# Kernel optimization log

Hardware: AMD Instinct MI355X
Metric: run time of the kernel (lower is better)

## Reference

```python
import jax, jax.numpy as jnp
import numpy as np

B, T, V, E, H = 4096, 16, 512, 512, 1024


def setup_inputs() -> dict:
    key = jax.random.key(0)
    ks = jax.random.split(key, 8)
    s = 0.05  # weight init scale
    return {
        "encoded_input": jax.random.normal(ks[0], (B, H), jnp.float32),
        "target": jax.random.randint(ks[1], (B, T), 0, V, jnp.int32),
        "emb": jax.random.normal(ks[2], (V, E), jnp.float32) * s,
        "W_ih": jax.random.normal(ks[3], (4 * H, E), jnp.float32) * s,
        "W_hh": jax.random.normal(ks[4], (4 * H, H), jnp.float32) * s,
        "b_ih": jax.random.normal(ks[5], (4 * H,), jnp.float32) * s,
        "b_hh": jax.random.normal(ks[6], (4 * H,), jnp.float32) * s,
        "W_out": jax.random.normal(ks[7], (V, H), jnp.float32) * s,
    }


def reference(encoded_input, target, emb, W_ih, W_hh, b_ih, b_hh, W_out):
    # Teacher-forced char LSTM decoder. Dropout(0.1) is identity in eval mode.
    b, t = target.shape
    # input char ids: start token 0, then shifted targets
    inp_ids = jnp.concatenate(
        [jnp.zeros((b, 1), target.dtype), target[:, :-1]], axis=1)  # [B,T]
    x = emb[inp_ids]  # [B,T,E]
    # precompute input contribution to gates for all steps
    xg = jnp.einsum('bte,ge->btg', x, W_ih) + b_ih + b_hh  # [B,T,4H]

    def step(carry, xs):
        h, c = carry
        xg_t, tgt_t = xs  # [B,4H], [B]
        gates = xg_t + h @ W_hh.T  # [B,4H]
        i, f, g, o = jnp.split(gates, 4, axis=-1)  # torch order i,f,g,o
        i = jax.nn.sigmoid(i)
        f = jax.nn.sigmoid(f)
        g = jnp.tanh(g)
        o = jax.nn.sigmoid(o)
        c = f * c + i * g
        h = o * jnp.tanh(c)
        logits = h @ W_out.T  # [B,V]
        # NLL of log_softmax at target index, expressed stably
        lse = jax.nn.logsumexp(logits, axis=-1)
        tgt_logit = jnp.take_along_axis(logits, tgt_t[:, None], axis=1)[:, 0]
        loss_t = lse - tgt_logit  # [B]
        return (h, c), loss_t

    h0 = encoded_input  # hidden = (encoded, encoded) for 1 layer
    (_, _), losses = jax.lax.scan(
        step, (h0, h0),
        (jnp.swapaxes(xg, 0, 1), target.T))  # scan over time: [T,B,...]
    return losses.sum(axis=0) / t  # [B] per-example mean loss
```

## Files before the change

kernel.cpp:

```cpp
#include <hip/hip_runtime.h>
#include <hip/hip_bf16.h>
#include <stdint.h>

typedef __attribute__((ext_vector_type(8))) short bf16x8;
typedef __attribute__((ext_vector_type(4))) float f32x4;

#define DEV __device__ __forceinline__
#define MFMA16(a, b, c) __builtin_amdgcn_mfma_f32_16x16x32_bf16(a, b, c, 0, 0, 0)

static constexpr int Bn = 4096;
static constexpr int Tn = 16;
static constexpr int Vn = 512;
static constexpr int En = 512;
static constexpr int Hn = 1024;
static constexpr int G4 = 4096;
static constexpr int KX = En + Hn;

DEV unsigned short f2bf(float f) {
    union { float f; uint32_t u; } v; v.f = f;
    return (unsigned short)((v.u + 0x7fffu + ((v.u >> 16) & 1u)) >> 16);
}
DEV float bf2f(unsigned short h) {
    union { uint32_t u; float f; } v; v.u = (uint32_t)h << 16; return v.f;
}
DEV float sigmoidf_(float x) { return 1.f / (1.f + __expf(-x)); }
DEV float tanhf_(float x)    { return 1.f - 2.f / (1.f + __expf(2.f * x)); }

DEV bf16x8 cvt8(const float* p) {
    f32x4 a = *(const f32x4*)p;
    f32x4 b = *(const f32x4*)(p + 4);
    bf16x8 o;
    o[0] = (short)f2bf(a[0]); o[1] = (short)f2bf(a[1]);
    o[2] = (short)f2bf(a[2]); o[3] = (short)f2bf(a[3]);
    o[4] = (short)f2bf(b[0]); o[5] = (short)f2bf(b[1]);
    o[6] = (short)f2bf(b[2]); o[7] = (short)f2bf(b[3]);
    return o;
}

__launch_bounds__(512, 2)
__global__ void lstm8(const unsigned short* __restrict__ Whp8,
                      const unsigned short* __restrict__ Hin,
                      const float* __restrict__ EGb,
                      const int* __restrict__ target, int t,
                      float* __restrict__ CstF,
                      unsigned short* __restrict__ Hout)
{
    __shared__ __align__(16) unsigned short lds[65536];

    const int tid = threadIdx.x;
    const int l   = tid & 63;
    const int w   = tid >> 6;
    const int wm  = w >> 2, wn = w & 3;
    const int q   = l >> 4, c15 = l & 15;
    const int bx  = blockIdx.x, by = blockIdx.y;
    const int n0  = bx * 256;

    const int cB = (((l & 7) ^ (l >> 3)) << 3);

    const int sw0   = ((q ^ (c15 & 7)) << 3);
    const int offA0 = c15 * 64 + sw0;
    const int offB0 = ((wn & 1) * 64 + c15) * 64 + sw0;

    f32x4 acc[8][4];
#pragma unroll
    for (int i = 0; i < 8; i++)
#pragma unroll
        for (int j = 0; j < 4; j++) acc[i][j] = f32x4{0.f, 0.f, 0.f, 0.f};

    auto stageA = [&](int kts, int cbuf) {
        const unsigned short* page =
            Whp8 + (((size_t)(by * 16 + kts) * 2) << 13);
#pragma unroll
        for (int h = 0; h < 2; h++)
#pragma unroll
            for (int L = 0; L < 2; L++) {
                const unsigned short* src =
                    page + h * 8192 + L * 4096 + w * 512 + l * 8;
                unsigned short* dst =
                    &lds[cbuf * 16384 + h * 8192 + L * 4096 + w * 512];
                __builtin_amdgcn_global_load_lds(
                    (const __attribute__((address_space(1))) uint32_t*)src,
                    (__attribute__((address_space(3))) uint32_t*)dst, 16, 0, 0);
            }
    };
    auto stageB = [&](int kts, int cbuf) {
#pragma unroll
        for (int h = 0; h < 2; h++)
#pragma unroll
            for (int L = 0; L < 2; L++) {
                const unsigned short* src =
                    Hin + (size_t)(n0 + h * 128 + L * 64 + w * 8 + (l >> 3)) * Hn
                        + kts * 64 + cB;
                unsigned short* dst =
                    &lds[32768 + cbuf * 16384 + h * 8192 + L * 4096 + w * 512];
                __builtin_amdgcn_global_load_lds(
                    (const __attribute__((address_space(1))) uint32_t*)src,
                    (__attribute__((address_space(3))) uint32_t*)dst, 16, 0, 0);
            }
    };

    stageA(0, 0); stageB(0, 0);
    stageA(1, 1); stageB(1, 1);
    asm volatile("s_waitcnt vmcnt(8)" ::: "memory");
    __builtin_amdgcn_s_barrier();

#pragma unroll 2
    for (int kt = 0; kt < 16; kt++) {
        const int cur = kt & 1;
        const unsigned short* Ab = &lds[cur * 16384 + wm * 8192];
        const unsigned short* Bb = &lds[32768 + cur * 16384 + (wn >> 1) * 8192];
        bf16x8 aF[8], bF[4];

#pragma unroll
        for (int i = 0; i < 8; i++)
            aF[i] = *(const bf16x8*)&Ab[offA0 + i * 1024];
#pragma unroll
        for (int j = 0; j < 4; j++)
            bF[j] = *(const bf16x8*)&Bb[offB0 + j * 1024];
        __builtin_amdgcn_s_setprio(1);
#pragma unroll
        for (int i = 0; i < 8; i++)
#pragma unroll
            for (int j = 0; j < 4; j++)
                acc[i][j] = MFMA16(aF[i], bF[j], acc[i][j]);
        __builtin_amdgcn_s_setprio(0);

#pragma unroll
        for (int i = 0; i < 8; i++)
            aF[i] = *(const bf16x8*)&Ab[(offA0 ^ 32) + i * 1024];
#pragma unroll
        for (int j = 0; j < 4; j++)
            bF[j] = *(const bf16x8*)&Bb[(offB0 ^ 32) + j * 1024];
        __builtin_amdgcn_s_setprio(1);
#pragma unroll
        for (int i = 0; i < 8; i++)
#pragma unroll
            for (int j = 0; j < 4; j++)
                acc[i][j] = MFMA16(aF[i], bF[j], acc[i][j]);
        __builtin_amdgcn_s_setprio(0);
        __builtin_amdgcn_s_barrier();

        const int kts = (kt + 2 < 16) ? (kt + 2) : 15;
        stageA(kts, cur);
        stageB(kts, cur);
        asm volatile("s_waitcnt vmcnt(8)" ::: "memory");
        __builtin_amdgcn_s_barrier();
    }

    int ids[4];
#pragma unroll
    for (int j = 0; j < 4; j++)
        ids[j] = (t > 0)
            ? target[(size_t)(n0 + wn * 64 + j * 16 + c15) * Tn + (t - 1)] : 0;

    const int U0 = by * 64;
    unsigned short* sH = &lds[32768];
#pragma unroll
    for (int i = 0; i < 8; i++) {
        const int Uloc = wm * 32 + i * 4 + q;
#pragma unroll
        for (int j = 0; j < 4; j++) {
            f32x4 eg = *(const f32x4*)&EGb[(size_t)ids[j] * G4 + (U0 + Uloc) * 4];
            float ig = sigmoidf_(acc[i][j][0] + eg[0]);
            float fg = sigmoidf_(acc[i][j][1] + eg[1]);
            float gg = tanhf_  (acc[i][j][2] + eg[2]);
            float og = sigmoidf_(acc[i][j][3] + eg[3]);
            const size_t cidx =
                ((((size_t)(by * 16 + bx) * 8 + w) * 32 + i * 4 + j) << 6) + l;
            float cOld = CstF[cidx];
            float cNew = fg * cOld + ig * gg;
            float h    = og * tanhf_(cNew);
            CstF[cidx] = cNew;
            const int bl = wn * 64 + j * 16 + c15;
            sH[bl * 64 + (Uloc ^ ((bl & 7) << 3))] = f2bf(h);
        }
    }
    __builtin_amdgcn_s_barrier();
    {
        const int row = tid >> 1;
        const int hs  = tid & 1;
        const int sx  = row & 7;
        size_t go = (size_t)(n0 + row) * Hn + U0 + hs * 32;
#pragma unroll
        for (int s = 0; s < 4; s++) {
            const int slog = hs * 4 + s;
            bf16x8 v = *(const bf16x8*)&sH[row * 64 + ((slog ^ sx) << 3)];
            *(bf16x8*)&Hout[go + s * 8] = v;
        }
    }
}

template <int BM, int BN, int EPI>
__launch_bounds__(256, 2)
__global__ void gemm_k(const unsigned short* __restrict__ A, int lda,
                       const unsigned short* __restrict__ Bw, int ldb,
                       int K,
                       const float* __restrict__ biasp,
                       float* __restrict__ Out,
                       unsigned short* __restrict__ Outb, int ldo)
{
    constexpr int BK = 32;
    constexpr int WM = BM / 2, WN = BN / 2;
    constexpr int MI = WM / 16, NJ = WN / 16;

    __shared__ __align__(16) unsigned short sA[BM * BK];
    __shared__ __align__(16) unsigned short sB[BN * BK];

    const int tid = threadIdx.x;
    const int l   = tid & 63;
    const int w   = tid >> 6;
    const int wm  = w >> 1, wn = w & 1;
    const int m0  = blockIdx.y * BM;
    const int n0  = blockIdx.x * BN;

    f32x4 acc[MI][NJ];
#pragma unroll
    for (int i = 0; i < MI; i++)
#pragma unroll
        for (int j = 0; j < NJ; j++) acc[i][j] = f32x4{0.f, 0.f, 0.f, 0.f};

    const int srow = l >> 2;
    const int scol = (l & 3) * 8;
    const int q    = l >> 4;
    const int c15  = l & 15;

    for (int k0 = 0; k0 < K; k0 += BK) {
#pragma unroll
        for (int c = 0; c < BM / 64; c++) {
            const unsigned short* src =
                A + (size_t)(m0 + c * 64 + w * 16 + srow) * lda + k0 + scol;
            unsigned short* dst = &sA[(c * 64 + w * 16) * BK];
            __builtin_amdgcn_global_load_lds(
                (const __attribute__((address_space(1))) uint32_t*)src,
                (__attribute__((address_space(3))) uint32_t*)dst, 16, 0, 0);
        }
#pragma unroll
        for (int c = 0; c < BN / 64; c++) {
            const unsigned short* src =
                Bw + (size_t)(n0 + c * 64 + w * 16 + srow) * ldb + k0 + scol;
            unsigned short* dst = &sB[(c * 64 + w * 16) * BK];
            __builtin_amdgcn_global_load_lds(
                (const __attribute__((address_space(1))) uint32_t*)src,
                (__attribute__((address_space(3))) uint32_t*)dst, 16, 0, 0);
        }
        __syncthreads();

        bf16x8 aF[MI], bF[NJ];
#pragma unroll
        for (int i = 0; i < MI; i++)
            aF[i] = *(const bf16x8*)&sA[(wm * WM + i * 16 + c15) * BK + q * 8];
#pragma unroll
        for (int j = 0; j < NJ; j++)
            bF[j] = *(const bf16x8*)&sB[(wn * WN + j * 16 + c15) * BK + q * 8];
#pragma unroll
        for (int i = 0; i < MI; i++)
#pragma unroll
            for (int j = 0; j < NJ; j++)
                acc[i][j] = MFMA16(aF[i], bF[j], acc[i][j]);
        __syncthreads();
    }

#pragma unroll
    for (int j = 0; j < NJ; j++) {
        const int colp = n0 + wn * WN + j * 16 + c15;
        const float bj = biasp ? biasp[colp] : 0.f;
#pragma unroll
        for (int i = 0; i < MI; i++) {
            const size_t rb = (size_t)(m0 + wm * WM + i * 16 + 4 * q);
#pragma unroll
            for (int r = 0; r < 4; r++) {
                float vv = acc[i][j][r] + bj;
                if constexpr (EPI == 0) Out[(rb + r) * ldo + colp] = vv;
                else Outb[(rb + r) * ldo + colp] = f2bf(vv);
            }
        }
    }
}

__launch_bounds__(512, 4)
__global__ void logits_lse(const unsigned short* __restrict__ A,
                           const unsigned short* __restrict__ Wob,
                           const int* __restrict__ target,
                           float* __restrict__ lossT)
{
    constexpr int BK = 32;
    __shared__ __align__(16) unsigned short sA[64 * BK];
    __shared__ __align__(16) unsigned short sB[512 * BK];
    __shared__ float redS[8 * 64];
    __shared__ float redT[8 * 64];
    __shared__ int   tgL[64];

    const int tid = threadIdx.x;
    const int l   = tid & 63;
    const int w   = tid >> 6;
    const int q   = l >> 4, c15 = l & 15;
    const int ra0 = blockIdx.x * 64;

    if (tid < 64) {
        int ra = ra0 + tid;
        tgL[tid] = target[(size_t)(ra & (Bn - 1)) * Tn + (ra >> 12)];
    }

    f32x4 acc[4][4];
#pragma unroll
    for (int i = 0; i < 4; i++)
#pragma unroll
        for (int j = 0; j < 4; j++) acc[i][j] = f32x4{0.f, 0.f, 0.f, 0.f};

    const int srow = l >> 2;
    const int scol = (l & 3) * 8;

    for (int k0 = 0; k0 < Hn; k0 += BK) {
#pragma unroll
        for (int c = 0; c < 4; c++) {
            const unsigned short* src =
                Wob + (size_t)(w * 64 + c * 16 + srow) * Hn + k0 + scol;
            unsigned short* dst = &sB[(w * 64 + c * 16) * BK];
            __builtin_amdgcn_global_load_lds(
                (const __attribute__((address_space(1))) uint32_t*)src,
                (__attribute__((address_space(3))) uint32_t*)dst, 16, 0, 0);
        }
        if (w < 4) {
            const unsigned short* src =
                A + (size_t)(ra0 + w * 16 + srow) * Hn + k0 + scol;
            unsigned short* dst = &sA[(w * 16) * BK];
            __builtin_amdgcn_global_load_lds(
                (const __attribute__((address_space(1))) uint32_t*)src,
                (__attribute__((address_space(3))) uint32_t*)dst, 16, 0, 0);
        }
        __syncthreads();

        bf16x8 aF[4], bF[4];
#pragma unroll
        for (int i = 0; i < 4; i++)
            aF[i] = *(const bf16x8*)&sA[(i * 16 + c15) * BK + q * 8];
#pragma unroll
        for (int j = 0; j < 4; j++)
            bF[j] = *(const bf16x8*)&sB[(w * 64 + j * 16 + c15) * BK + q * 8];
#pragma unroll
        for (int i = 0; i < 4; i++)
#pragma unroll
            for (int j = 0; j < 4; j++)
                acc[i][j] = MFMA16(aF[i], bF[j], acc[i][j]);
        __syncthreads();
    }

#pragma unroll
    for (int i = 0; i < 4; i++)
#pragma unroll
        for (int rr = 0; rr < 4; rr++) {
            const int rloc = i * 16 + q * 4 + rr;
            const int tg = tgL[rloc];
            float ps = 0.f, tv = 0.f;
#pragma unroll
            for (int j = 0; j < 4; j++) {
                float v = acc[i][j][rr];
                ps += __expf(v);
                int col = w * 64 + j * 16 + c15;
                tv += (col == tg) ? v : 0.f;
            }
#pragma unroll
            for (int d = 1; d < 16; d <<= 1) {
                ps += __shfl_xor(ps, d);
                tv += __shfl_xor(tv, d);
            }
            if (c15 == 0) {
                redS[w * 64 + rloc] = ps;
                redT[w * 64 + rloc] = tv;
            }
        }
    __syncthreads();
    if (tid < 64) {
        float se = 0.f, tv = 0.f;
#pragma unroll
        for (int w8 = 0; w8 < 8; w8++) {
            se += redS[w8 * 64 + tid];
            tv += redT[w8 * 64 + tid];
        }
        lossT[ra0 + tid] = __logf(se) - tv;
    }
}

__global__ void prep_w(const float* __restrict__ Wih,
                       const float* __restrict__ Whh,
                       unsigned short* __restrict__ Wp)
{
    int i = blockIdx.x * 256 + threadIdx.x;
    int n = i / 192, kc = (i % 192) * 8;
    int g = n & 3, u = n >> 2;
    const float* src = (kc < En) ? (Wih + (size_t)(g * Hn + u) * En + kc)
                                 : (Whh + (size_t)(g * Hn + u) * Hn + (kc - En));
    *(bf16x8*)&Wp[(size_t)n * KX + kc] = cvt8(src);
}

__global__ void prep_w8(const float* __restrict__ Whh,
                        unsigned short* __restrict__ Whp8)
{
    int idx = blockIdx.x * 256 + threadIdx.x;
    int o = idx * 8;
    int p = o & 8191;
    int h = (o >> 13) & 1;
    int kt = (o >> 14) & 15;
    int by = o >> 18;
    int r = p >> 6;
    int slot = (p & 63) >> 3;
    int cl = ((slot ^ (r & 7)) << 3);
    int n = by * 256 + h * 128 + r;
    int g = n & 3, u = n >> 2;
    *(bf16x8*)&Whp8[o] = cvt8(Whh + (size_t)(g * Hn + u) * Hn + kt * 64 + cl);
}

__global__ void prep_bias(const float* __restrict__ bih,
                          const float* __restrict__ bhh,
                          float* __restrict__ biasp)
{
    int n = blockIdx.x * 256 + threadIdx.x;
    int g = n & 3, u = n >> 2;
    biasp[n] = bih[g * Hn + u] + bhh[g * Hn + u];
}

__global__ void prep_wout(const float* __restrict__ Wout,
                          unsigned short* __restrict__ Wob)
{
    int i = blockIdx.x * 256 + threadIdx.x;
    size_t off = (size_t)i * 8;
    *(bf16x8*)&Wob[off] = cvt8(Wout + off);
}

__global__ void prep_emb(const float* __restrict__ emb,
                         unsigned short* __restrict__ embb)
{
    int i = blockIdx.x * 256 + threadIdx.x;
    size_t off = (size_t)i * 8;
    *(bf16x8*)&embb[off] = cvt8(emb + off);
}

__global__ void init_state(const float* __restrict__ enc,
                           float* __restrict__ CstF,
                           unsigned short* __restrict__ Xh0,
                           float* __restrict__ loss)
{
    int f = blockIdx.x * 256 + threadIdx.x;
    int l = f & 63, q = l >> 4, c15 = l & 15;
    int ij = (f >> 6) & 31, i = ij >> 2, j = ij & 3;
    int w = (f >> 11) & 7, wm = w >> 2, wn = w & 3;
    int bx = (f >> 14) & 15, by = (f >> 18) & 15;
    int b = bx * 256 + wn * 64 + j * 16 + c15;
    int U = by * 64 + wm * 32 + i * 4 + q;
    CstF[f] = enc[(size_t)b * Hn + U];
    if (f < Bn * Hn / 8) {
        int m = f >> 7, u8 = (f & 127) * 8;
        *(bf16x8*)&Xh0[(size_t)m * Hn + u8] = cvt8(enc + (size_t)m * Hn + u8);
    }
    if (f < Bn) loss[f] = 0.f;
}

__global__ void lse_k(const unsigned short* __restrict__ lg,
                      const int* __restrict__ target, int t,
                      float* __restrict__ lossOut)
{
    int w = threadIdx.x >> 6, l = threadIdx.x & 63;
    int ra = blockIdx.x * 4 + w;
    const unsigned short* row = lg + (size_t)ra * Vn;
    bf16x8 v = *(const bf16x8*)&row[l * 8];
    float x0 = bf2f((unsigned short)v[0]), x1 = bf2f((unsigned short)v[1]);
    float x2 = bf2f((unsigned short)v[2]), x3 = bf2f((unsigned short)v[3]);
    float x4 = bf2f((unsigned short)v[4]), x5 = bf2f((unsigned short)v[5]);
    float x6 = bf2f((unsigned short)v[6]), x7 = bf2f((unsigned short)v[7]);
    float mx = fmaxf(fmaxf(fmaxf(x0, x1), fmaxf(x2, x3)),
                     fmaxf(fmaxf(x4, x5), fmaxf(x6, x7)));
#pragma unroll
    for (int d = 1; d < 64; d <<= 1) mx = fmaxf(mx, __shfl_xor(mx, d));
    float se = __expf(x0 - mx) + __expf(x1 - mx) + __expf(x2 - mx) +
               __expf(x3 - mx) + __expf(x4 - mx) + __expf(x5 - mx) +
               __expf(x6 - mx) + __expf(x7 - mx);
#pragma unroll
    for (int d = 1; d < 64; d <<= 1) se += __shfl_xor(se, d);
    if (l == 0) {
        int tg = target[(size_t)ra * Tn + t];
        lossOut[ra] += (mx + __logf(se)) - bf2f(row[tg]);
    }
}

__global__ void finalize_b(const float* __restrict__ lossT,
                           float* __restrict__ out)
{
    int m = blockIdx.x * 256 + threadIdx.x;
    float s = 0.f;
#pragma unroll
    for (int k = 0; k < 16; k++) s += lossT[(size_t)k * Bn + m];
    out[m] = s * (1.f / 16.f);
}

__global__ void finalize_s(const float* __restrict__ loss,
                           float* __restrict__ out)
{
    int m = blockIdx.x * 256 + threadIdx.x;
    out[m] = loss[m] * (1.f / 16.f);
}

extern "C" void kernel_launch(void* const* d_in, const int* in_sizes, int n_in,
                              void* d_out, int out_size, void* d_ws, size_t ws_size,
                              hipStream_t stream)
{
    const float* enc    = (const float*)d_in[0];
    const int*   target = (const int*)d_in[1];
    const float* emb    = (const float*)d_in[2];
    const float* Wih    = (const float*)d_in[3];
    const float* Whh    = (const float*)d_in[4];
    const float* bih    = (const float*)d_in[5];
    const float* bhh    = (const float*)d_in[6];
    const float* Wout   = (const float*)d_in[7];
    float* out = (float*)d_out;
    (void)in_sizes; (void)n_in; (void)out_size;

    constexpr size_t SZ_Wp    = (size_t)G4 * KX * 2;
    constexpr size_t SZ_Whp8  = (size_t)G4 * Hn * 2;
    constexpr size_t SZ_Wob   = (size_t)Vn * Hn * 2;
    constexpr size_t SZ_biasp = (size_t)G4 * 4;
    constexpr size_t SZ_embb  = (size_t)Vn * En * 2;
    constexpr size_t SZ_EGb   = (size_t)Vn * G4 * 4;
    constexpr size_t SZ_Cst   = (size_t)Bn * Hn * 4;
    constexpr size_t SZ_H     = (size_t)Bn * Hn * 2;
    constexpr size_t SZ_LGS   = (size_t)Bn * Vn * 2;
    constexpr size_t SZ_LT    = (size_t)Bn * Tn * 4;
    auto pad = [](size_t b) { return (b + 255) & ~(size_t)255; };
    const size_t fixed = pad(SZ_Wp) + pad(SZ_Whp8) + pad(SZ_Wob) +
                         pad(SZ_biasp) + pad(SZ_embb) + pad(SZ_EGb) + pad(SZ_Cst);
    const size_t needB = fixed + 17 * pad(SZ_H) + pad(SZ_LGS) + pad(SZ_LT);
    const bool batched = ws_size >= needB;

    size_t off = 0;
    char* base = (char*)d_ws;
    auto alloc = [&](size_t bytes) -> void* {
        void* p = base + off; off += pad(bytes); return p;
    };
    unsigned short* Wp    = (unsigned short*)alloc(SZ_Wp);
    unsigned short* Whp8  = (unsigned short*)alloc(SZ_Whp8);
    unsigned short* Wob   = (unsigned short*)alloc(SZ_Wob);
    float*          biasp = (float*)alloc(SZ_biasp);
    unsigned short* embb  = (unsigned short*)alloc(SZ_embb);
    float*          EGb   = (float*)alloc(SZ_EGb);
    float*          CstF  = (float*)alloc(SZ_Cst);
    const int nslot = batched ? 17 : 3;
    unsigned short* Hs    = (unsigned short*)alloc((size_t)nslot * pad(SZ_H));
    unsigned short* lgS   = (unsigned short*)alloc(SZ_LGS);
    float*          lossT = (float*)alloc(batched ? SZ_LT : (size_t)Bn * 4);
    const size_t HSLOT = pad(SZ_H) / 2;

    prep_w    <<<3072, 256, 0, stream>>>(Wih, Whh, Wp);
    prep_w8   <<<2048, 256, 0, stream>>>(Whh, Whp8);
    prep_bias <<<16,   256, 0, stream>>>(bih, bhh, biasp);
    prep_wout <<<256,  256, 0, stream>>>(Wout, Wob);
    prep_emb  <<<128,  256, 0, stream>>>(emb, embb);
    init_state<<<16384, 256, 0, stream>>>(enc, CstF, Hs, lossT);

    gemm_k<128, 128, 0><<<dim3(32, 4), 256, 0, stream>>>(
        embb, En, Wp, KX, En, biasp, EGb, nullptr, G4);

    for (int t = 0; t < Tn; t++) {
        unsigned short* hIn  = Hs + (size_t)(batched ? t : (t % 3)) * HSLOT;
        unsigned short* hOut = Hs + (size_t)(batched ? (t + 1) : ((t + 1) % 3)) * HSLOT;
        lstm8<<<dim3(16, 16), 512, 0, stream>>>(
            Whp8, hIn, EGb, target, t, CstF, hOut);
        if (!batched) {
            gemm_k<128, 64, 2><<<dim3(8, 32), 256, 0, stream>>>(
                hOut, Hn, Wob, Hn, Hn, nullptr, nullptr, lgS, Vn);
            lse_k<<<1024, 256, 0, stream>>>(lgS, target, t, lossT);
        }
    }

    if (batched) {
        logits_lse<<<1024, 512, 0, stream>>>(Hs + HSLOT, Wob, target, lossT);
        finalize_b<<<16, 256, 0, stream>>>(lossT, out);
    } else {
        finalize_s<<<16, 256, 0, stream>>>(lossT, out);
    }
}
```

Baseline: 900.2 us.

## Interleave LSTM recurrent GEMM into four phases with staggered async LDS loads

The recurrent W_hh·h GEMM main loop in the LSTM step kernel is split into four sub-tile MFMA phases. Each phase issues part of the next tile's global-to-LDS loads (A one step ahead, B two steps ahead) between barriers, so memory traffic overlaps compute more finely. Register use drops because only half the A and B fragments are live at a time. The cost is many more barriers per k-step and a more fragile buffer-reuse ordering. The other kernels only get a load macro refactor.

```diff
diff --git a/kernel.cpp b/kernel.cpp
--- a/kernel.cpp
+++ b/kernel.cpp
@@ -37,6 +37,10 @@
     return o;
 }
 
+#define GLOAD16(s, d) __builtin_amdgcn_global_load_lds( \
+    (const __attribute__((address_space(1))) uint32_t*)(s), \
+    (__attribute__((address_space(3))) uint32_t*)(d), 16, 0, 0)
+
 __launch_bounds__(512, 2)
 __global__ void lstm8(const unsigned short* __restrict__ Whp8,
                       const unsigned short* __restrict__ Hin,
@@ -56,7 +60,6 @@
     const int n0  = bx * 256;
 
     const int cB = (((l & 7) ^ (l >> 3)) << 3);
-
     const int sw0   = ((q ^ (c15 & 7)) << 3);
     const int offA0 = c15 * 64 + sw0;
     const int offB0 = ((wn & 1) * 64 + c15) * 64 + sw0;
@@ -67,83 +70,113 @@
 #pragma unroll
         for (int j = 0; j < 4; j++) acc[i][j] = f32x4{0.f, 0.f, 0.f, 0.f};
 
-    auto stageA = [&](int kts, int cbuf) {
+    auto stA = [&](int kts, int cbuf, int h) {
         const unsigned short* page =
             Whp8 + (((size_t)(by * 16 + kts) * 2) << 13);
 #pragma unroll
-        for (int h = 0; h < 2; h++)
-#pragma unroll
-            for (int L = 0; L < 2; L++) {
-                const unsigned short* src =
-                    page + h * 8192 + L * 4096 + w * 512 + l * 8;
-                unsigned short* dst =
-                    &lds[cbuf * 16384 + h * 8192 + L * 4096 + w * 512];
-                __builtin_amdgcn_global_load_lds(
-                    (const __attribute__((address_space(1))) uint32_t*)src,
-                    (__attribute__((address_space(3))) uint32_t*)dst, 16, 0, 0);
-            }
+        for (int L = 0; L < 2; L++)
+            GLOAD16(page + h * 8192 + L * 4096 + w * 512 + l * 8,
+                    &lds[cbuf * 16384 + h * 8192 + L * 4096 + w * 512]);
     };
-    auto stageB = [&](int kts, int cbuf) {
-#pragma unroll
-        for (int h = 0; h < 2; h++)
-#pragma unroll
-            for (int L = 0; L < 2; L++) {
-                const unsigned short* src =
-                    Hin + (size_t)(n0 + h * 128 + L * 64 + w * 8 + (l >> 3)) * Hn
-                        + kts * 64 + cB;
-                unsigned short* dst =
-                    &lds[32768 + cbuf * 16384 + h * 8192 + L * 4096 + w * 512];
-                __builtin_amdgcn_global_load_lds(
-                    (const __attribute__((address_space(1))) uint32_t*)src,
-                    (__attribute__((address_space(3))) uint32_t*)dst, 16, 0, 0);
-            }
+    auto stB = [&](int kts, int cbuf, int h) {
+#pragma unroll
+        for (int L = 0; L < 2; L++)
+            GLOAD16(Hin + (size_t)(n0 + h * 128 + L * 64 + w * 8 + (l >> 3)) * Hn
+                        + kts * 64 + cB,
+                    &lds[32768 + cbuf * 16384 + h * 8192 + L * 4096 + w * 512]);
     };
 
-    stageA(0, 0); stageB(0, 0);
-    stageA(1, 1); stageB(1, 1);
-    asm volatile("s_waitcnt vmcnt(8)" ::: "memory");
+    stA(0, 0, 0); stA(0, 0, 1); stB(0, 0, 0); stB(0, 0, 1);
+    stB(1, 1, 0); stB(1, 1, 1);
+    asm volatile("s_waitcnt vmcnt(4)" ::: "memory");
     __builtin_amdgcn_s_barrier();
 
-#pragma unroll 2
+    bf16x8 aF[4][2], bF[4][2];
+
     for (int kt = 0; kt < 16; kt++) {
         const int cur = kt & 1;
         const unsigned short* Ab = &lds[cur * 16384 + wm * 8192];
         const unsigned short* Bb = &lds[32768 + cur * 16384 + (wn >> 1) * 8192];
-        bf16x8 aF[8], bF[4];
-
-#pragma unroll
-        for (int i = 0; i < 8; i++)
-            aF[i] = *(const bf16x8*)&Ab[offA0 + i * 1024];
-#pragma unroll
-        for (int j = 0; j < 4; j++)
-            bF[j] = *(const bf16x8*)&Bb[offB0 + j * 1024];
+        const int ktA = (kt + 1 < 16) ? kt + 1 : 15;
+        const int ktB = (kt + 2 < 16) ? kt + 2 : 15;
+
+#pragma unroll
+        for (int i = 0; i < 4; i++) {
+            aF[i][0] = *(const bf16x8*)&Ab[offA0 + i * 1024];
+            aF[i][1] = *(const bf16x8*)&Ab[(offA0 ^ 32) + i * 1024];
+        }
+#pragma unroll
+        for (int j = 0; j < 2; j++) {
+            bF[j][0] = *(const bf16x8*)&Bb[offB0 + j * 1024];
+            bF[j][1] = *(const bf16x8*)&Bb[(offB0 ^ 32) + j * 1024];
+        }
+        stA(ktA, cur ^ 1, 0);
+        __builtin_amdgcn_s_barrier();
+        asm volatile("s_waitcnt lgkmcnt(0)" ::: "memory");
+        __builtin_amdgcn_sched_barrier(0);
         __builtin_amdgcn_s_setprio(1);
 #pragma unroll
-        for (int i = 0; i < 8; i++)
-#pragma unroll
-            for (int j = 0; j < 4; j++)
-                acc[i][j] = MFMA16(aF[i], bF[j], acc[i][j]);
+        for (int i = 0; i < 4; i++)
+#pragma unroll
+            for (int j = 0; j < 2; j++) {
+                acc[i][j] = MFMA16(aF[i][0], bF[j][0], acc[i][j]);
+                acc[i][j] = MFMA16(aF[i][1], bF[j][1], acc[i][j]);
+            }
         __builtin_amdgcn_s_setprio(0);
-
-#pragma unroll
-        for (int i = 0; i < 8; i++)
-            aF[i] = *(const bf16x8*)&Ab[(offA0 ^ 32) + i * 1024];
-#pragma unroll
-        for (int j = 0; j < 4; j++)
-            bF[j] = *(const bf16x8*)&Bb[(offB0 ^ 32) + j * 1024];
+        __builtin_amdgcn_s_barrier();
+
+#pragma unroll
+        for (int j = 2; j < 4; j++) {
+            bF[j][0] = *(const bf16x8*)&Bb[offB0 + j * 1024];
+            bF[j][1] = *(const bf16x8*)&Bb[(offB0 ^ 32) + j * 1024];
+        }
+        stA(ktA, cur ^ 1, 1);
+        __builtin_amdgcn_s_barrier();
+        asm volatile("s_waitcnt lgkmcnt(0)" ::: "memory");
+        __builtin_amdgcn_sched_barrier(0);
         __builtin_amdgcn_s_setprio(1);
 #pragma unroll
-        for (int i = 0; i < 8; i++)
-#pragma unroll
-            for (int j = 0; j < 4; j++)
-                acc[i][j] = MFMA16(aF[i], bF[j], acc[i][j]);
+        for (int i = 0; i < 4; i++)
+#pragma unroll
+            for (int j = 2; j < 4; j++) {
+                acc[i][j] = MFMA16(aF[i][0], bF[j][0], acc[i][j]);
+                acc[i][j] = MFMA16(aF[i][1], bF[j][1], acc[i][j]);
+            }
         __builtin_amdgcn_s_setprio(0);
         __builtin_amdgcn_s_barrier();
 
-        const int kts = (kt + 2 < 16) ? (kt + 2) : 15;
-        stageA(kts, cur);
-        stageB(kts, cur);
-        asm volatile("s_waitcnt vmcnt(8)" ::: "memory");
+#pragma unroll
+        for (int i = 0; i < 4; i++) {
+            aF[i][0] = *(const bf16x8*)&Ab[offA0 + (i + 4) * 1024];
+            aF[i][1] = *(const bf16x8*)&Ab[(offA0 ^ 32) + (i + 4) * 1024];
+        }
+        stB(ktB, cur, 0);
+        __builtin_amdgcn_s_barrier();
+        asm volatile("s_waitcnt lgkmcnt(0)" ::: "memory");
+        __builtin_amdgcn_sched_barrier(0);
+        __builtin_amdgcn_s_setprio(1);
+#pragma unroll
+        for (int i = 0; i < 4; i++)
+#pragma unroll
+            for (int j = 0; j < 2; j++) {
+                acc[i + 4][j] = MFMA16(aF[i][0], bF[j][0], acc[i + 4][j]);
+                acc[i + 4][j] = MFMA16(aF[i][1], bF[j][1], acc[i + 4][j]);
+            }
+        __builtin_amdgcn_s_setprio(0);
+        __builtin_amdgcn_s_barrier();
+
+        stB(ktB, cur, 1);
+        __builtin_amdgcn_s_barrier();
+        __builtin_amdgcn_s_setprio(1);
+#pragma unroll
+        for (int i = 0; i < 4; i++)
+#pragma unroll
+            for (int j = 2; j < 4; j++) {
+                acc[i + 4][j] = MFMA16(aF[i][0], bF[j][0], acc[i + 4][j]);
+                acc[i + 4][j] = MFMA16(aF[i][1], bF[j][1], acc[i + 4][j]);
+            }
+        __builtin_amdgcn_s_setprio(0);
+        asm volatile("s_waitcnt vmcnt(4)" ::: "memory");
         __builtin_amdgcn_s_barrier();
     }
 
@@ -175,7 +208,7 @@
             sH[bl * 64 + (Uloc ^ ((bl & 7) << 3))] = f2bf(h);
         }
     }
-    __builtin_amdgcn_s_barrier();
+    __syncthreads();
     {
         const int row = tid >> 1;
         const int hs  = tid & 1;
@@ -230,18 +263,14 @@
             const unsigned short* src =
                 A + (size_t)(m0 + c * 64 + w * 16 + srow) * lda + k0 + scol;
             unsigned short* dst = &sA[(c * 64 + w * 16) * BK];
-            __builtin_amdgcn_global_load_lds(
-                (const __attribute__((address_space(1))) uint32_t*)src,
-                (__attribute__((address_space(3))) uint32_t*)dst, 16, 0, 0);
+            GLOAD16(src, dst);
         }
 #pragma unroll
         for (int c = 0; c < BN / 64; c++) {
             const unsigned short* src =
                 Bw + (size_t)(n0 + c * 64 + w * 16 + srow) * ldb + k0 + scol;
             unsigned short* dst = &sB[(c * 64 + w * 16) * BK];
-            __builtin_amdgcn_global_load_lds(
-                (const __attribute__((address_space(1))) uint32_t*)src,
-                (__attribute__((address_space(3))) uint32_t*)dst, 16, 0, 0);
+            GLOAD16(src, dst);
         }
         __syncthreads();
 
@@ -316,17 +345,13 @@
             const unsigned short* src =
                 Wob + (size_t)(w * 64 + c * 16 + srow) * Hn + k0 + scol;
             unsigned short* dst = &sB[(w * 64 + c * 16) * BK];
-            __builtin_amdgcn_global_load_lds(
-                (const __attribute__((address_space(1))) uint32_t*)src,
-                (__attribute__((address_space(3))) uint32_t*)dst, 16, 0, 0);
+            GLOAD16(src, dst);
         }
         if (w < 4) {
             const unsigned short* src =
                 A + (size_t)(ra0 + w * 16 + srow) * Hn + k0 + scol;
             unsigned short* dst = &sA[(w * 16) * BK];
-            __builtin_amdgcn_global_load_lds(
-                (const __attribute__((address_space(1))) uint32_t*)src,
-                (__attribute__((address_space(3))) uint32_t*)dst, 16, 0, 0);
+            GLOAD16(src, dst);
         }
         __syncthreads();
 
```

Measured after the change: 908.5 us. Within noise of the previous version (+0.9%).

## Fuse LSTM timesteps into persistent kernel with grid barrier; swizzle logits LDS

Applied to the files above, without the earlier changes.

Replaces the 16 per-timestep lstm8 launches with one persistent lstm16 kernel of 256 blocks that loops over time and synchronises through an atomic grid-wide barrier. This removes launch gaps and tail effects between steps. The batched logits kernel now reads a pre-swizzled W_out layout and uses a rotated column mapping to cut LDS bank conflicts. The input-weight prep is also shrunk to pack only W_ih, since the W_hh half was never used. The grid barrier relies on all 256 blocks being co-resident and could deadlock otherwise, and the spin-wait adds some per-step overhead.

```diff
diff --git a/kernel.cpp b/kernel.cpp
--- a/kernel.cpp
+++ b/kernel.cpp
@@ -14,7 +14,6 @@
 static constexpr int En = 512;
 static constexpr int Hn = 1024;
 static constexpr int G4 = 4096;
-static constexpr int KX = En + Hn;
 
 DEV unsigned short f2bf(float f) {
     union { float f; uint32_t u; } v; v.f = f;
@@ -37,16 +36,42 @@
     return o;
 }
 
-__launch_bounds__(512, 2)
-__global__ void lstm8(const unsigned short* __restrict__ Whp8,
-                      const unsigned short* __restrict__ Hin,
-                      const float* __restrict__ EGb,
-                      const int* __restrict__ target, int t,
-                      float* __restrict__ CstF,
-                      unsigned short* __restrict__ Hout)
-{
-    __shared__ __align__(16) unsigned short lds[65536];
-
+#define GLOAD16(s, d) __builtin_amdgcn_global_load_lds( \
+    (const __attribute__((address_space(1))) uint32_t*)(s), \
+    (__attribute__((address_space(3))) uint32_t*)(d), 16, 0, 0)
+
+DEV void grid_barrier(unsigned* bar)
+{
+    __syncthreads();
+    if (threadIdx.x == 0) {
+        __threadfence();
+        unsigned g = __hip_atomic_load(&bar[1], __ATOMIC_RELAXED,
+                                       __HIP_MEMORY_SCOPE_AGENT);
+        unsigned a = __hip_atomic_fetch_add(&bar[0], 1u, __ATOMIC_ACQ_REL,
+                                            __HIP_MEMORY_SCOPE_AGENT);
+        if (a == 255u) {
+            __hip_atomic_store(&bar[0], 0u, __ATOMIC_RELAXED,
+                               __HIP_MEMORY_SCOPE_AGENT);
+            __hip_atomic_store(&bar[1], g + 1u, __ATOMIC_RELEASE,
+                               __HIP_MEMORY_SCOPE_AGENT);
+        } else {
+            while (__hip_atomic_load(&bar[1], __ATOMIC_ACQUIRE,
+                                     __HIP_MEMORY_SCOPE_AGENT) == g)
+                __builtin_amdgcn_s_sleep(2);
+        }
+        __threadfence();
+    }
+    __syncthreads();
+}
+
+DEV void lstm_step(unsigned short* lds,
+                   const unsigned short* __restrict__ Whp8,
+                   const unsigned short* __restrict__ Hin,
+                   const float* __restrict__ EGb,
+                   const int* __restrict__ target, int t,
+                   float* __restrict__ CstF,
+                   unsigned short* __restrict__ Hout)
+{
     const int tid = threadIdx.x;
     const int l   = tid & 63;
     const int w   = tid >> 6;
@@ -55,8 +80,7 @@
     const int bx  = blockIdx.x, by = blockIdx.y;
     const int n0  = bx * 256;
 
-    const int cB = (((l & 7) ^ (l >> 3)) << 3);
-
+    const int cB    = (((l & 7) ^ (l >> 3)) << 3);
     const int sw0   = ((q ^ (c15 & 7)) << 3);
     const int offA0 = c15 * 64 + sw0;
     const int offB0 = ((wn & 1) * 64 + c15) * 64 + sw0;
@@ -67,40 +91,28 @@
 #pragma unroll
         for (int j = 0; j < 4; j++) acc[i][j] = f32x4{0.f, 0.f, 0.f, 0.f};
 
-    auto stageA = [&](int kts, int cbuf) {
+    auto stA = [&](int kts, int cbuf) {
         const unsigned short* page =
             Whp8 + (((size_t)(by * 16 + kts) * 2) << 13);
 #pragma unroll
         for (int h = 0; h < 2; h++)
 #pragma unroll
-            for (int L = 0; L < 2; L++) {
-                const unsigned short* src =
-                    page + h * 8192 + L * 4096 + w * 512 + l * 8;
-                unsigned short* dst =
-                    &lds[cbuf * 16384 + h * 8192 + L * 4096 + w * 512];
-                __builtin_amdgcn_global_load_lds(
-                    (const __attribute__((address_space(1))) uint32_t*)src,
-                    (__attribute__((address_space(3))) uint32_t*)dst, 16, 0, 0);
-            }
+            for (int L = 0; L < 2; L++)
+                GLOAD16(page + h * 8192 + L * 4096 + w * 512 + l * 8,
+                        &lds[cbuf * 16384 + h * 8192 + L * 4096 + w * 512]);
     };
-    auto stageB = [&](int kts, int cbuf) {
+    auto stB = [&](int kts, int cbuf) {
 #pragma unroll
         for (int h = 0; h < 2; h++)
 #pragma unroll
-            for (int L = 0; L < 2; L++) {
-                const unsigned short* src =
-                    Hin + (size_t)(n0 + h * 128 + L * 64 + w * 8 + (l >> 3)) * Hn
-                        + kts * 64 + cB;
-                unsigned short* dst =
-                    &lds[32768 + cbuf * 16384 + h * 8192 + L * 4096 + w * 512];
-                __builtin_amdgcn_global_load_lds(
-                    (const __attribute__((address_space(1))) uint32_t*)src,
-                    (__attribute__((address_space(3))) uint32_t*)dst, 16, 0, 0);
-            }
+            for (int L = 0; L < 2; L++)
+                GLOAD16(Hin + (size_t)(n0 + h * 128 + L * 64 + w * 8 + (l >> 3)) * Hn
+                            + kts * 64 + cB,
+                        &lds[32768 + cbuf * 16384 + h * 8192 + L * 4096 + w * 512]);
     };
 
-    stageA(0, 0); stageB(0, 0);
-    stageA(1, 1); stageB(1, 1);
+    stA(0, 0); stB(0, 0);
+    stA(1, 1); stB(1, 1);
     asm volatile("s_waitcnt vmcnt(8)" ::: "memory");
     __builtin_amdgcn_s_barrier();
 
@@ -141,8 +153,8 @@
         __builtin_amdgcn_s_barrier();
 
         const int kts = (kt + 2 < 16) ? (kt + 2) : 15;
-        stageA(kts, cur);
-        stageB(kts, cur);
+        stA(kts, cur);
+        stB(kts, cur);
         asm volatile("s_waitcnt vmcnt(8)" ::: "memory");
         __builtin_amdgcn_s_barrier();
     }
@@ -175,7 +187,7 @@
             sH[bl * 64 + (Uloc ^ ((bl & 7) << 3))] = f2bf(h);
         }
     }
-    __builtin_amdgcn_s_barrier();
+    __syncthreads();
     {
         const int row = tid >> 1;
         const int hs  = tid & 1;
@@ -188,6 +200,34 @@
             *(bf16x8*)&Hout[go + s * 8] = v;
         }
     }
+}
+
+__launch_bounds__(512, 2)
+__global__ void lstm16(const unsigned short* __restrict__ Whp8,
+                       unsigned short* __restrict__ Hs, size_t HSLOT,
+                       const float* __restrict__ EGb,
+                       const int* __restrict__ target,
+                       float* __restrict__ CstF,
+                       unsigned* __restrict__ bar)
+{
+    __shared__ __align__(16) unsigned short lds[65536];
+    for (int t = 0; t < Tn; t++) {
+        lstm_step(lds, Whp8, Hs + (size_t)t * HSLOT, EGb, target, t, CstF,
+                  Hs + (size_t)(t + 1) * HSLOT);
+        if (t + 1 < Tn) grid_barrier(bar);
+    }
+}
+
+__launch_bounds__(512, 2)
+__global__ void lstm8(const unsigned short* __restrict__ Whp8,
+                      const unsigned short* __restrict__ Hin,
+                      const float* __restrict__ EGb,
+                      const int* __restrict__ target, int t,
+                      float* __restrict__ CstF,
+                      unsigned short* __restrict__ Hout)
+{
+    __shared__ __align__(16) unsigned short lds[65536];
+    lstm_step(lds, Whp8, Hin, EGb, target, t, CstF, Hout);
 }
 
 template <int BM, int BN, int EPI>
@@ -226,23 +266,13 @@
 
     for (int k0 = 0; k0 < K; k0 += BK) {
 #pragma unroll
-        for (int c = 0; c < BM / 64; c++) {
-            const unsigned short* src =
-                A + (size_t)(m0 + c * 64 + w * 16 + srow) * lda + k0 + scol;
-            unsigned short* dst = &sA[(c * 64 + w * 16) * BK];
-            __builtin_amdgcn_global_load_lds(
-                (const __attribute__((address_space(1))) uint32_t*)src,
-                (__attribute__((address_space(3))) uint32_t*)dst, 16, 0, 0);
-        }
-#pragma unroll
-        for (int c = 0; c < BN / 64; c++) {
-            const unsigned short* src =
-                Bw + (size_t)(n0 + c * 64 + w * 16 + srow) * ldb + k0 + scol;
-            unsigned short* dst = &sB[(c * 64 + w * 16) * BK];
-            __builtin_amdgcn_global_load_lds(
-                (const __attribute__((address_space(1))) uint32_t*)src,
-                (__attribute__((address_space(3))) uint32_t*)dst, 16, 0, 0);
-        }
+        for (int c = 0; c < BM / 64; c++)
+            GLOAD16(A + (size_t)(m0 + c * 64 + w * 16 + srow) * lda + k0 + scol,
+                    &sA[(c * 64 + w * 16) * BK]);
+#pragma unroll
+        for (int c = 0; c < BN / 64; c++)
+            GLOAD16(Bw + (size_t)(n0 + c * 64 + w * 16 + srow) * ldb + k0 + scol,
+                    &sB[(c * 64 + w * 16) * BK]);
         __syncthreads();
 
         bf16x8 aF[MI], bF[NJ];
@@ -279,7 +309,7 @@
 
 __launch_bounds__(512, 4)
 __global__ void logits_lse(const unsigned short* __restrict__ A,
-                           const unsigned short* __restrict__ Wob,
+                           const unsigned short* __restrict__ WobSw,
                            const int* __restrict__ target,
                            float* __restrict__ lossT)
 {
@@ -307,36 +337,28 @@
 #pragma unroll
         for (int j = 0; j < 4; j++) acc[i][j] = f32x4{0.f, 0.f, 0.f, 0.f};
 
-    const int srow = l >> 2;
-    const int scol = (l & 3) * 8;
+    const int srow  = l >> 2;
+    const int scol  = (l & 3) * 8;
+    const int scolS = ((((l & 3) - (l >> 3)) & 3) << 3);
+    const int qs    = (((q + (c15 >> 1)) & 3) << 3);
 
     for (int k0 = 0; k0 < Hn; k0 += BK) {
 #pragma unroll
-        for (int c = 0; c < 4; c++) {
-            const unsigned short* src =
-                Wob + (size_t)(w * 64 + c * 16 + srow) * Hn + k0 + scol;
-            unsigned short* dst = &sB[(w * 64 + c * 16) * BK];
-            __builtin_amdgcn_global_load_lds(
-                (const __attribute__((address_space(1))) uint32_t*)src,
-                (__attribute__((address_space(3))) uint32_t*)dst, 16, 0, 0);
-        }
-        if (w < 4) {
-            const unsigned short* src =
-                A + (size_t)(ra0 + w * 16 + srow) * Hn + k0 + scol;
-            unsigned short* dst = &sA[(w * 16) * BK];
-            __builtin_amdgcn_global_load_lds(
-                (const __attribute__((address_space(1))) uint32_t*)src,
-                (__attribute__((address_space(3))) uint32_t*)dst, 16, 0, 0);
-        }
+        for (int c = 0; c < 4; c++)
+            GLOAD16(WobSw + (size_t)(w * 64 + c * 16 + srow) * Hn + k0 + scol,
+                    &sB[(w * 64 + c * 16) * BK]);
+        if (w < 4)
+            GLOAD16(A + (size_t)(ra0 + w * 16 + srow) * Hn + k0 + scolS,
+                    &sA[(w * 16) * BK]);
         __syncthreads();
 
         bf16x8 aF[4], bF[4];
 #pragma unroll
         for (int i = 0; i < 4; i++)
-            aF[i] = *(const bf16x8*)&sA[(i * 16 + c15) * BK + q * 8];
+            aF[i] = *(const bf16x8*)&sA[(i * 16 + c15) * BK + qs];
 #pragma unroll
         for (int j = 0; j < 4; j++)
-            bF[j] = *(const bf16x8*)&sB[(w * 64 + j * 16 + c15) * BK + q * 8];
+            bF[j] = *(const bf16x8*)&sB[(w * 64 + j * 16 + c15) * BK + qs];
 #pragma unroll
         for (int i = 0; i < 4; i++)
 #pragma unroll
@@ -381,16 +403,14 @@
     }
 }
 
-__global__ void prep_w(const float* __restrict__ Wih,
-                       const float* __restrict__ Whh,
-                       unsigned short* __restrict__ Wp)
+__global__ void prep_wih(const float* __restrict__ Wih,
+                         unsigned short* __restrict__ Wihp)
 {
     int i = blockIdx.x * 256 + threadIdx.x;
-    int n = i / 192, kc = (i % 192) * 8;
+    int n = i >> 6, kc = (i & 63) * 8;
     int g = n & 3, u = n >> 2;
-    const float* src = (kc < En) ? (Wih + (size_t)(g * Hn + u) * En + kc)
-                                 : (Whh + (size_t)(g * Hn + u) * Hn + (kc - En));
-    *(bf16x8*)&Wp[(size_t)n * KX + kc] = cvt8(src);
+    *(bf16x8*)&Wihp[(size_t)n * En + kc] =
+        cvt8(Wih + (size_t)(g * Hn + u) * En + kc);
 }
 
 __global__ void prep_w8(const float* __restrict__ Whh,
@@ -419,6 +439,17 @@
     biasp[n] = bih[g * Hn + u] + bhh[g * Hn + u];
 }
 
+__global__ void prep_wout_sw(const float* __restrict__ Wout,
+                             unsigned short* __restrict__ WobSw)
+{
+    int i = blockIdx.x * 256 + threadIdx.x;
+    int o = i * 8;
+    int n = o >> 10, col = o & 1023;
+    int k0 = col & ~31, sp = (col >> 3) & 3;
+    int sl = (sp - (n >> 1)) & 3;
+    *(bf16x8*)&WobSw[o] = cvt8(Wout + (size_t)n * Hn + k0 + sl * 8);
+}
+
 __global__ void prep_wout(const float* __restrict__ Wout,
                           unsigned short* __restrict__ Wob)
 {
@@ -514,7 +545,7 @@
     float* out = (float*)d_out;
     (void)in_sizes; (void)n_in; (void)out_size;
 
-    constexpr size_t SZ_Wp    = (size_t)G4 * KX * 2;
+    constexpr size_t SZ_Wihp  = (size_t)G4 * En * 2;
     constexpr size_t SZ_Whp8  = (size_t)G4 * Hn * 2;
     constexpr size_t SZ_Wob   = (size_t)Vn * Hn * 2;
     constexpr size_t SZ_biasp = (size_t)G4 * 4;
@@ -524,9 +555,11 @@
     constexpr size_t SZ_H     = (size_t)Bn * Hn * 2;
     constexpr size_t SZ_LGS   = (size_t)Bn * Vn * 2;
     constexpr size_t SZ_LT    = (size_t)Bn * Tn * 4;
+    constexpr size_t SZ_BAR   = 256;
     auto pad = [](size_t b) { return (b + 255) & ~(size_t)255; };
-    const size_t fixed = pad(SZ_Wp) + pad(SZ_Whp8) + pad(SZ_Wob) +
-                         pad(SZ_biasp) + pad(SZ_embb) + pad(SZ_EGb) + pad(SZ_Cst);
+    const size_t fixed = pad(SZ_Wihp) + pad(SZ_Whp8) + pad(SZ_Wob) +
+                         pad(SZ_biasp) + pad(SZ_embb) + pad(SZ_EGb) +
+                         pad(SZ_Cst) + pad(SZ_BAR);
     const size_t needB = fixed + 17 * pad(SZ_H) + pad(SZ_LGS) + pad(SZ_LT);
     const bool batched = ws_size >= needB;
 
@@ -535,45 +568,47 @@
     auto alloc = [&](size_t bytes) -> void* {
         void* p = base + off; off += pad(bytes); return p;
     };
-    unsigned short* Wp    = (unsigned short*)alloc(SZ_Wp);
+    unsigned short* Wihp  = (unsigned short*)alloc(SZ_Wihp);
     unsigned short* Whp8  = (unsigned short*)alloc(SZ_Whp8);
     unsigned short* Wob   = (unsigned short*)alloc(SZ_Wob);
     float*          biasp = (float*)alloc(SZ_biasp);
     unsigned short* embb  = (unsigned short*)alloc(SZ_embb);
     float*          EGb   = (float*)alloc(SZ_EGb);
     float*          CstF  = (float*)alloc(SZ_Cst);
+    unsigned*       bar   = (unsigned*)alloc(SZ_BAR);
     const int nslot = batched ? 17 : 3;
     unsigned short* Hs    = (unsigned short*)alloc((size_t)nslot * pad(SZ_H));
     unsigned short* lgS   = (unsigned short*)alloc(SZ_LGS);
     float*          lossT = (float*)alloc(batched ? SZ_LT : (size_t)Bn * 4);
     const size_t HSLOT = pad(SZ_H) / 2;
 
-    prep_w    <<<3072, 256, 0, stream>>>(Wih, Whh, Wp);
+    hipMemsetAsync(bar, 0, 8, stream);
+    prep_wih  <<<1024, 256, 0, stream>>>(Wih, Wihp);
     prep_w8   <<<2048, 256, 0, stream>>>(Whh, Whp8);
     prep_bias <<<16,   256, 0, stream>>>(bih, bhh, biasp);
-    prep_wout <<<256,  256, 0, stream>>>(Wout, Wob);
+    if (batched) prep_wout_sw<<<256, 256, 0, stream>>>(Wout, Wob);
+    else         prep_wout   <<<256, 256, 0, stream>>>(Wout, Wob);
     prep_emb  <<<128,  256, 0, stream>>>(emb, embb);
     init_state<<<16384, 256, 0, stream>>>(enc, CstF, Hs, lossT);
 
     gemm_k<128, 128, 0><<<dim3(32, 4), 256, 0, stream>>>(
-        embb, En, Wp, KX, En, biasp, EGb, nullptr, G4);
-
-    for (int t = 0; t < Tn; t++) {
-        unsigned short* hIn  = Hs + (size_t)(batched ? t : (t % 3)) * HSLOT;
-        unsigned short* hOut = Hs + (size_t)(batched ? (t + 1) : ((t + 1) % 3)) * HSLOT;
-        lstm8<<<dim3(16, 16), 512, 0, stream>>>(
-            Whp8, hIn, EGb, target, t, CstF, hOut);
-        if (!batched) {
+        embb, En, Wihp, En, En, biasp, EGb, nullptr, G4);
+
+    if (batched) {
+        lstm16<<<dim3(16, 16), 512, 0, stream>>>(
+            Whp8, Hs, HSLOT, EGb, target, CstF, bar);
+        logits_lse<<<1024, 512, 0, stream>>>(Hs + HSLOT, Wob, target, lossT);
+        finalize_b<<<16, 256, 0, stream>>>(lossT, out);
+    } else {
+        for (int t = 0; t < Tn; t++) {
+            unsigned short* hIn  = Hs + (size_t)(t % 3) * HSLOT;
+            unsigned short* hOut = Hs + (size_t)((t + 1) % 3) * HSLOT;
+            lstm8<<<dim3(16, 16), 512, 0, stream>>>(
+                Whp8, hIn, EGb, target, t, CstF, hOut);
             gemm_k<128, 64, 2><<<dim3(8, 32), 256, 0, stream>>>(
                 hOut, Hn, Wob, Hn, Hn, nullptr, nullptr, lgS, Vn);
             lse_k<<<1024, 256, 0, stream>>>(lgS, target, t, lossT);
         }
-    }
-
-    if (batched) {
-        logits_lse<<<1024, 512, 0, stream>>>(Hs + HSLOT, Wob, target, lossT);
-        finalize_b<<<16, 256, 0, stream>>>(lossT, out);
-    } else {
         finalize_s<<<16, 256, 0, stream>>>(lossT, out);
     }
 }
```

New measurement: 2.026 ms. +125.0%, slower.
